# Performance work log

Hardware: AMD Instinct MI355X
Metric: run time of the kernel (lower is better)

## Reference

```python
import jax, jax.numpy as jnp
import numpy as np

B, S, C, HD = 1, 2048, 2048, 128
H = C // HD  # 16 heads
EPS = float(jnp.finfo(jnp.float32).eps)  # torch nn.RMSNorm default eps


def setup_inputs() -> dict:
    key = jax.random.key(0)
    ks = jax.random.split(key, 10)
    std = 1.0 / np.sqrt(C)
    return {
        "x": jax.random.normal(ks[0], (B, S, C), jnp.float32),
        "rope": jax.random.normal(ks[1], (1, S, 1, HD // 2, 2, 2), jnp.float32),
        "wq": jax.random.normal(ks[2], (C, C), jnp.float32) * std,
        "bq": jax.random.normal(ks[3], (C,), jnp.float32) * 0.01,
        "wk": jax.random.normal(ks[4], (C, C), jnp.float32) * std,
        "bk": jax.random.normal(ks[5], (C,), jnp.float32) * 0.01,
        "wv": jax.random.normal(ks[6], (C, C), jnp.float32) * std,
        "bv": jax.random.normal(ks[7], (C,), jnp.float32) * 0.01,
        "q_norm_w": jnp.ones((HD,), jnp.float32),
        "k_norm_w": jnp.ones((HD,), jnp.float32),
        "wo": jax.random.normal(ks[8], (C, C), jnp.float32) * std,
        "bo": jax.random.normal(ks[9], (C,), jnp.float32) * 0.01,
    }


def _rmsnorm(x, w):
    # x: [..., HD]
    ms = jnp.mean(x * x, axis=-1, keepdims=True)
    return x * jax.lax.rsqrt(ms + EPS) * w


def _apply_rotary(x, rope):
    # x: [B,S,H,HD]; rope: [1,S,1,HD//2,2,2]
    shp = x.shape
    x_ = x.reshape(*shp[:-1], -1, 1, 2)          # [B,S,H,HD/2,1,2]
    out = (rope * x_).sum(axis=-1)               # [B,S,H,HD/2,2]
    return out.reshape(shp)


def reference(x, rope, wq, bq, wk, bk, wv, bv, q_norm_w, k_norm_w, wo, bo):
    q = x @ wq.T + bq
    k = x @ wk.T + bk
    v = x @ wv.T + bv
    q = q.reshape(B, S, H, HD)
    k = k.reshape(B, S, H, HD)
    v = v.reshape(B, S, H, HD)
    q = _rmsnorm(q, q_norm_w)
    k = _rmsnorm(k, k_norm_w)
    q = _apply_rotary(q, rope)
    k = _apply_rotary(k, rope)
    scale = 1.0 / np.sqrt(HD)
    scores = jnp.einsum("bqhd,bkhd->bhqk", q, k) * scale  # [B,H,S,S]
    attn = jax.nn.softmax(scores, axis=-1)
    out = jnp.einsum("bhqk,bkhd->bqhd", attn, v).reshape(B, S, C)
    return out @ wo.T + bo
```

## Files before the change

### kernel.cpp

```cpp
#include <hip/hip_runtime.h>
#include <stdint.h>

#define GLOBAL_AS __attribute__((address_space(1)))
#define LDS_AS    __attribute__((address_space(3)))

typedef unsigned short u16;
typedef __attribute__((ext_vector_type(8))) __bf16 bf16x8;
typedef __attribute__((ext_vector_type(4))) float   f32x4;
typedef __attribute__((ext_vector_type(2))) float   f32x2;
typedef __attribute__((ext_vector_type(4))) u16     u16x4;

#if __has_builtin(__builtin_amdgcn_exp2f)
#define EXP2(x) __builtin_amdgcn_exp2f(x)
#else
#define EXP2(x) __exp2f(x)
#endif

static __device__ __forceinline__ float bf2f(u16 u) {
    union { uint32_t i; float f; } c; c.i = ((uint32_t)u) << 16; return c.f;
}
static __device__ __forceinline__ u16 f2bf(float f) {
    union { float f; uint32_t i; } c; c.f = f;
    uint32_t r = c.i + 0x7fffu + ((c.i >> 16) & 1u);
    return (u16)(r >> 16);
}
static __device__ __forceinline__ u16 f2bf_fast(float f) {
    union { float f; uint32_t i; } c; c.f = f;
    return (u16)((c.i + 0x8000u) >> 16);
}
static __device__ __forceinline__ void gl_lds16(const void* g, void* l) {
    __builtin_amdgcn_global_load_lds((GLOBAL_AS const uint32_t*)g,
                                     (LDS_AS uint32_t*)l, 16, 0, 0);
}
static __device__ __forceinline__ f32x4 mfma16(bf16x8 a, bf16x8 b, f32x4 c) {
    return __builtin_amdgcn_mfma_f32_16x16x32_bf16(a, b, c, 0, 0, 0);
}

__global__ __launch_bounds__(256) void cast5(
    const float* __restrict__ s0, const float* __restrict__ s1,
    const float* __restrict__ s2, const float* __restrict__ s3,
    const float* __restrict__ s4,
    u16* __restrict__ d0, u16* __restrict__ d1, u16* __restrict__ d2,
    u16* __restrict__ d3, u16* __restrict__ d4)
{
    const float* s; u16* d;
    switch (blockIdx.y) {
        case 0: s = s0; d = d0; break;
        case 1: s = s1; d = d1; break;
        case 2: s = s2; d = d2; break;
        case 3: s = s3; d = d3; break;
        default: s = s4; d = d4; break;
    }
    int i = (blockIdx.x * 256 + threadIdx.x) * 4;
    f32x4 v = *(const f32x4*)&s[i];
    u16x4 u = { f2bf(v[0]), f2bf(v[1]), f2bf(v[2]), f2bf(v[3]) };
    *(u16x4*)&d[i] = u;
}

__global__ __launch_bounds__(512, 2) void gemm_qkv7(
    const u16* __restrict__ x,
    const u16* __restrict__ wq, const u16* __restrict__ wk, const u16* __restrict__ wv,
    const float* __restrict__ bq, const float* __restrict__ bk, const float* __restrict__ bv,
    u16* __restrict__ q, u16* __restrict__ k, u16* __restrict__ v)
{
    __shared__ u16 SL[4][16384];
    const int tid = threadIdx.x, l = tid & 63, w = tid >> 6;
    const int wm = w >> 2, wn = w & 3;
    const int lr = l & 15, lg = l >> 4;
    const int lg2 = lg ^ ((lr >> 1) & 3);
    const int bid = blockIdx.x;
    const int bm = bid & 7, bn = bid >> 3;

    const u16* Ab = x + (size_t)(bm * 256) * 2048;

    const int uA0 = tid,       rA0 = uA0 >> 2, cA0 = (uA0 & 3) ^ ((rA0 >> 1) & 3);
    const int uA1 = 512 + tid, rA1 = uA1 >> 2, cA1 = (uA1 & 3) ^ ((rA1 >> 1) & 3);
    const u16* apA0 = Ab + (size_t)rA0 * 2048 + cA0 * 8;
    const u16* apA1 = Ab + (size_t)rA1 * 2048 + cA1 * 8;
    const int ub0 = tid;
    int ub1 = 512 + tid; if (ub1 > 767) ub1 = 767;
    const int rB0 = ub0 >> 2, cB0 = (ub0 & 3) ^ ((rB0 >> 1) & 3);
    const int rB1 = ub1 >> 2, cB1 = (ub1 & 3) ^ ((rB1 >> 1) & 3);
    const int gr0 = bn * 192 + rB0, gr1 = bn * 192 + rB1;
    const u16* base0 = gr0 < 2048 ? wq : (gr0 < 4096 ? wk : wv);
    const u16* base1 = gr1 < 2048 ? wq : (gr1 < 4096 ? wk : wv);
    const u16* bpB0 = base0 + (size_t)(gr0 & 2047) * 2048 + cB0 * 8;
    const u16* bpB1 = base1 + (size_t)(gr1 & 2047) * 2048 + cB1 * 8;
    const int dA0 = uA0 * 8, dA1 = uA1 * 8;
    const int dB0 = (1024 + tid) * 8, dB1 = (1536 + tid) * 8;

    auto stageA = [&](u16* slot) {
        gl_lds16(apA0, slot + dA0);
        gl_lds16(apA1, slot + dA1);
        apA0 += 32; apA1 += 32;
    };
    auto stageB = [&](u16* slot) {
        gl_lds16(bpB0, slot + dB0);
        gl_lds16(bpB1, slot + dB1);
        bpB0 += 32; bpB1 += 32;
    };

    f32x4 acc[8][3];
#pragma unroll
    for (int mi = 0; mi < 8; ++mi)
#pragma unroll
        for (int nj = 0; nj < 3; ++nj) acc[mi][nj] = (f32x4){0.f, 0.f, 0.f, 0.f};

    stageA((u16*)SL[0]); stageB((u16*)SL[0]);
    stageA((u16*)SL[1]); stageB((u16*)SL[1]);
    stageA((u16*)SL[2]); stageB((u16*)SL[2]);

    const int ar = wm * 128 + lr;
    const int br = wn * 48 + lr;

    auto iter_body = [&](const u16* As0, const u16* As1, u16* sl3, u16* sl4) {
        const u16* Bs0 = As0 + 8192;
        const u16* Bs1 = As1 + 8192;

        asm volatile("s_waitcnt vmcnt(4)" ::: "memory");
        __builtin_amdgcn_s_barrier();
        __builtin_amdgcn_sched_barrier(0);

        bf16x8 b0[3], alo0[4], ahi0[4], b1[3], alo1[4], ahi1[4];

        stageA(sl3);
#pragma unroll
        for (int nj = 0; nj < 3; ++nj)
            b0[nj] = *(const bf16x8*)&Bs0[(br + nj * 16) * 32 + lg2 * 8];
#pragma unroll
        for (int mi = 0; mi < 4; ++mi)
            alo0[mi] = *(const bf16x8*)&As0[(ar + mi * 16) * 32 + lg2 * 8];
#pragma unroll
        for (int mi = 0; mi < 4; ++mi)
            ahi0[mi] = *(const bf16x8*)&As0[(ar + (4 + mi) * 16) * 32 + lg2 * 8];
        __builtin_amdgcn_s_setprio(1);
#pragma unroll
        for (int mi = 0; mi < 4; ++mi)
#pragma unroll
            for (int nj = 0; nj < 3; ++nj)
                acc[mi][nj] = mfma16(alo0[mi], b0[nj], acc[mi][nj]);
        __builtin_amdgcn_s_setprio(0);

        stageB(sl3);
#pragma unroll
        for (int nj = 0; nj < 3; ++nj)
            b1[nj] = *(const bf16x8*)&Bs1[(br + nj * 16) * 32 + lg2 * 8];
#pragma unroll
        for (int mi = 0; mi < 4; ++mi)
            alo1[mi] = *(const bf16x8*)&As1[(ar + mi * 16) * 32 + lg2 * 8];
        __builtin_amdgcn_s_setprio(1);
#pragma unroll
        for (int mi = 0; mi < 4; ++mi)
#pragma unroll
            for (int nj = 0; nj < 3; ++nj)
                acc[4 + mi][nj] = mfma16(ahi0[mi], b0[nj], acc[4 + mi][nj]);
        __builtin_amdgcn_s_setprio(0);

        __builtin_amdgcn_sched_barrier(0);
        __builtin_amdgcn_s_barrier();
        __builtin_amdgcn_sched_barrier(0);

        stageA(sl4);
#pragma unroll
        for (int mi = 0; mi < 4; ++mi)
            ahi1[mi] = *(const bf16x8*)&As1[(ar + (4 + mi) * 16) * 32 + lg2 * 8];
        __builtin_amdgcn_s_setprio(1);
#pragma unroll
        for (int mi = 0; mi < 4; ++mi)
#pragma unroll
            for (int nj = 0; nj < 3; ++nj)
                acc[mi][nj] = mfma16(alo1[mi], b1[nj], acc[mi][nj]);
        __builtin_amdgcn_s_setprio(0);

        stageB(sl4);
        __builtin_amdgcn_s_setprio(1);
#pragma unroll
        for (int mi = 0; mi < 4; ++mi)
#pragma unroll
            for (int nj = 0; nj < 3; ++nj)
                acc[4 + mi][nj] = mfma16(ahi1[mi], b1[nj], acc[4 + mi][nj]);
        __builtin_amdgcn_s_setprio(0);
    };

#pragma unroll 1
    for (int it2 = 0; it2 < 16; ++it2) {
        iter_body((const u16*)SL[0], (const u16*)SL[1], (u16*)SL[3], (u16*)SL[0]);
        iter_body((const u16*)SL[2], (const u16*)SL[3], (u16*)SL[1], (u16*)SL[2]);
    }
    asm volatile("s_waitcnt vmcnt(0)" ::: "memory");

#pragma unroll
    for (int mi = 0; mi < 8; ++mi) {
        int row0 = bm * 256 + wm * 128 + mi * 16 + lg * 4;
#pragma unroll
        for (int nj = 0; nj < 3; ++nj) {
            int col = bn * 192 + wn * 48 + nj * 16 + lr;
            int cs = (col >> 11), cc = col & 2047;
            u16* C = cs == 0 ? q : (cs == 1 ? k : v);
            const float* bp = cs == 0 ? bq : (cs == 1 ? bk : bv);
            float bs = bp[cc];
#pragma unroll
            for (int reg = 0; reg < 4; ++reg)
                C[(size_t)(row0 + reg) * 2048 + cc] = f2bf(acc[mi][nj][reg] + bs);
        }
    }
}

__global__ __launch_bounds__(256, 2) void gemm_out4(
    const u16* __restrict__ a, const u16* __restrict__ wo,
    const float* __restrict__ bo, float* __restrict__ out)
{
    __shared__ u16 SL[4][8192];
    const int tid = threadIdx.x, l = tid & 63, w = tid >> 6;
    const int wm = w >> 1, wn = w & 1;
    const int lr = l & 15, lg = l >> 4;
    const int lg2 = lg ^ ((lr >> 1) & 3);
    const int bid = blockIdx.x;
    const int xcd = bid & 7, j = bid >> 3;
    const int bm = xcd * 2 + (j & 1), bn = j >> 1;

    const u16* Ab = a  + (size_t)(bm * 128) * 2048;
    const u16* Bb = wo + (size_t)(bn * 128) * 2048;

    const int r0 = tid >> 2,        c0 = (tid & 3) ^ ((r0 >> 1) & 3);
    const int r1 = (256 + tid) >> 2, c1 = ((256 + tid) & 3) ^ ((r1 >> 1) & 3);
    const u16* apA0 = Ab + (size_t)r0 * 2048 + c0 * 8;
    const u16* apA1 = Ab + (size_t)r1 * 2048 + c1 * 8;
    const u16* bpB0 = Bb + (size_t)r0 * 2048 + c0 * 8;
    const u16* bpB1 = Bb + (size_t)r1 * 2048 + c1 * 8;
    const int dA0 = tid * 8, dA1 = (256 + tid) * 8;
    const int dB0 = (512 + tid) * 8, dB1 = (768 + tid) * 8;

    auto stage = [&](u16* slot) {
        gl_lds16(apA0, slot + dA0);
        gl_lds16(apA1, slot + dA1);
        gl_lds16(bpB0, slot + dB0);
        gl_lds16(bpB1, slot + dB1);
        apA0 += 32; apA1 += 32; bpB0 += 32; bpB1 += 32;
    };

    f32x4 acc[4][4];
#pragma unroll
    for (int mi = 0; mi < 4; ++mi)
#pragma unroll
        for (int nj = 0; nj < 4; ++nj) acc[mi][nj] = (f32x4){0.f, 0.f, 0.f, 0.f};

    stage((u16*)SL[0]); stage((u16*)SL[1]); stage((u16*)SL[2]);

    auto ob = [&](const u16* As, u16* sln) {
        const u16* Bs = As + 4096;
        asm volatile("s_waitcnt vmcnt(8)" ::: "memory");
        __builtin_amdgcn_s_barrier();
        __builtin_amdgcn_sched_barrier(0);

        stage(sln);

        bf16x8 bf[4], af0[2];
#pragma unroll
        for (int nj = 0; nj < 4; ++nj)
            bf[nj] = *(const bf16x8*)&Bs[(wn * 64 + nj * 16 + lr) * 32 + lg2 * 8];
#pragma unroll
        for (int mi = 0; mi < 2; ++mi)
            af0[mi] = *(const bf16x8*)&As[(wm * 64 + mi * 16 + lr) * 32 + lg2 * 8];
        __builtin_amdgcn_s_setprio(1);
#pragma unroll
        for (int mi = 0; mi < 2; ++mi)
#pragma unroll
            for (int nj = 0; nj < 4; ++nj)
                acc[mi][nj] = mfma16(af0[mi], bf[nj], acc[mi][nj]);
        __builtin_amdgcn_s_setprio(0);
        __builtin_amdgcn_s_barrier();
        __builtin_amdgcn_sched_barrier(0);

        bf16x8 af1[2];
#pragma unroll
        for (int mi = 0; mi < 2; ++mi)
            af1[mi] = *(const bf16x8*)&As[(wm * 64 + (2 + mi) * 16 + lr) * 32 + lg2 * 8];
        __builtin_amdgcn_s_setprio(1);
#pragma unroll
        for (int mi = 0; mi < 2; ++mi)
#pragma unroll
            for (int nj = 0; nj < 4; ++nj)
                acc[2 + mi][nj] = mfma16(af1[mi], bf[nj], acc[2 + mi][nj]);
        __builtin_amdgcn_s_setprio(0);
    };

#pragma unroll 1
    for (int it4 = 0; it4 < 16; ++it4) {
        ob((const u16*)SL[0], (u16*)SL[3]);
        ob((const u16*)SL[1], (u16*)SL[0]);
        ob((const u16*)SL[2], (u16*)SL[1]);
        ob((const u16*)SL[3], (u16*)SL[2]);
    }
    asm volatile("s_waitcnt vmcnt(0)" ::: "memory");

#pragma unroll
    for (int mi = 0; mi < 4; ++mi) {
        int row0 = bm * 128 + wm * 64 + mi * 16 + lg * 4;
#pragma unroll
        for (int nj = 0; nj < 4; ++nj) {
            int col = bn * 128 + wn * 64 + nj * 16 + lr;
            float bs = bo[col];
#pragma unroll
            for (int reg = 0; reg < 4; ++reg)
                out[(size_t)(row0 + reg) * 2048 + col] = acc[mi][nj][reg] + bs;
        }
    }
}

__global__ __launch_bounds__(256) void norm_rope(
    const u16* __restrict__ qb, const u16* __restrict__ kb,
    const float* __restrict__ rope, const float* __restrict__ qw, const float* __restrict__ kw,
    u16* __restrict__ qh, u16* __restrict__ kh)
{
    const int tid = threadIdx.x, l = tid & 63, w = tid >> 6;
    const int rowid = blockIdx.x * 4 + w;
    const int h = rowid & 15, s = rowid >> 4;
    const size_t gbase = (size_t)s * 2048 + h * 128 + 2 * l;

    uint32_t qu = *(const uint32_t*)&qb[gbase];
    uint32_t ku = *(const uint32_t*)&kb[gbase];
    float q0 = bf2f((u16)qu), q1 = bf2f((u16)(qu >> 16));
    float k0 = bf2f((u16)ku), k1 = bf2f((u16)(ku >> 16));

    float sq = q0 * q0 + q1 * q1;
    float sk = k0 * k0 + k1 * k1;
#pragma unroll
    for (int m = 1; m < 64; m <<= 1) {
        sq += __shfl_xor(sq, m);
        sk += __shfl_xor(sk, m);
    }
    const float EPS = 1.1920928955078125e-07f;
    const float SCALE = 0.08838834764831845f * 1.4426950408889634f;
    float rq = rsqrtf(sq * (1.f / 128.f) + EPS) * SCALE;
    float rk = rsqrtf(sk * (1.f / 128.f) + EPS);

    f32x2 wq2 = *(const f32x2*)&qw[2 * l];
    f32x2 wk2 = *(const f32x2*)&kw[2 * l];
    float qn0 = q0 * rq * wq2[0], qn1 = q1 * rq * wq2[1];
    float kn0 = k0 * rk * wk2[0], kn1 = k1 * rk * wk2[1];

    f32x4 rr = *(const f32x4*)&rope[(size_t)s * 256 + l * 4];
    float qo0 = rr[0] * qn0 + rr[1] * qn1;
    float qo1 = rr[2] * qn0 + rr[3] * qn1;
    float ko0 = rr[0] * kn0 + rr[1] * kn1;
    float ko1 = rr[2] * kn0 + rr[3] * kn1;

    const size_t obase = ((size_t)h * 2048 + s) * 128 + 2 * l;
    *(uint32_t*)&qh[obase] = (uint32_t)f2bf(qo0) | ((uint32_t)f2bf(qo1) << 16);
    *(uint32_t*)&kh[obase] = (uint32_t)f2bf(ko0) | ((uint32_t)f2bf(ko1) << 16);
}

__global__ __launch_bounds__(256) void transpose_v(
    const u16* __restrict__ vb, u16* __restrict__ vt)
{
    __shared__ u16 t[64 * 80];
    const int h = blockIdx.z, s0 = blockIdx.x * 64, d0 = blockIdx.y * 64;
    const int tid = threadIdx.x;
#pragma unroll
    for (int cc = tid; cc < 512; cc += 256) {
        int r = cc >> 3, u = cc & 7;
        *(bf16x8*)&t[r * 80 + u * 8] =
            *(const bf16x8*)&vb[(size_t)(s0 + r) * 2048 + h * 128 + d0 + u * 8];
    }
    __syncthreads();
#pragma unroll
    for (int cc = tid; cc < 512; cc += 256) {
        int dr = cc >> 3, u = cc & 7;
        u16 vv[8];
#pragma unroll
        for (int j = 0; j < 8; ++j) vv[j] = t[(u * 8 + j) * 80 + dr];
        u16x4 lo = { vv[0], vv[1], vv[2], vv[3] };
        u16x4 hi = { vv[4], vv[5], vv[6], vv[7] };
        u16* dst = &vt[((size_t)h * 128 + d0 + dr) * 2048 + s0 + u * 8];
        *(u16x4*)dst = lo;
        *(u16x4*)(dst + 4) = hi;
    }
}

__global__ __launch_bounds__(256, 2) void attn(
    const u16* __restrict__ qh, const u16* __restrict__ kh,
    const u16* __restrict__ vt, u16* __restrict__ Opb, float* __restrict__ Lp)
{
    __shared__ u16 Ks[64 * 128];
    __shared__ u16 Vs[128 * 64];
    __shared__ u16 Ps[4][32 * 68];
    const int tid = threadIdx.x, l = tid & 63, w = tid >> 6;
    const int h = blockIdx.z, half = blockIdx.y;
    const int q0 = blockIdx.x * 128 + w * 32;
    const int lr = l & 15, lg = l >> 4;
    const float SHIFT = -17.312340490667562f;

    const u16* Kh = kh + (size_t)h * 2048 * 128;
    const u16* Vh = vt + (size_t)h * 128 * 2048;
    const int kvbase = half * 1024;

    bf16x8 qf[2][4];
#pragma unroll
    for (int am = 0; am < 2; ++am)
#pragma unroll
        for (int kk = 0; kk < 4; ++kk)
            qf[am][kk] = *(const bf16x8*)
                &qh[((size_t)h * 2048 + q0 + am * 16 + lr) * 128 + kk * 32 + lg * 8];

    bf16x8 onesf;
#pragma unroll
    for (int j = 0; j < 8; ++j) {
        union { u16 u; __bf16 b; } cb; cb.u = 0x3F80;
        onesf[j] = cb.b;
    }

    f32x4 o[2][8];
#pragma unroll
    for (int am = 0; am < 2; ++am)
#pragma unroll
        for (int dj = 0; dj < 8; ++dj) o[am][dj] = (f32x4){0.f, 0.f, 0.f, 0.f};
    f32x4 ol[2] = { (f32x4){0.f, 0.f, 0.f, 0.f}, (f32x4){0.f, 0.f, 0.f, 0.f} };

#pragma unroll 1
    for (int t = 0; t < 16; ++t) {
        const int kv0 = kvbase + t * 64;
        __syncthreads();
#pragma unroll
        for (int r = 0; r < 4; ++r) {
            int c = w * 4 + r;
            {
                int row = c * 4 + (l >> 4);
                int u = (l & 15) ^ (row & 7);
                gl_lds16(Kh + (size_t)(kv0 + row) * 128 + u * 8, &Ks[c * 512 + l * 8]);
            }
            {
                int row = c * 8 + (l >> 3);
                int u = (l & 7) ^ (row & 7);
                gl_lds16(Vh + (size_t)row * 2048 + kv0 + u * 8, &Vs[c * 512 + l * 8]);
            }
        }
        __syncthreads();

        f32x4 sc[2][4];
#pragma unroll
        for (int am = 0; am < 2; ++am)
#pragma unroll
            for (int nj = 0; nj < 4; ++nj)
                sc[am][nj] = (f32x4){SHIFT, SHIFT, SHIFT, SHIFT};
        __builtin_amdgcn_s_setprio(1);
#pragma unroll
        for (int kk = 0; kk < 4; ++kk)
#pragma unroll
            for (int nj = 0; nj < 4; ++nj) {
                int n = nj * 16 + lr;
                bf16x8 b = *(const bf16x8*)&Ks[n * 128 + ((kk * 4 + lg) ^ (n & 7)) * 8];
#pragma unroll
                for (int am = 0; am < 2; ++am)
                    sc[am][nj] = mfma16(qf[am][kk], b, sc[am][nj]);
            }
        __builtin_amdgcn_s_setprio(0);

#pragma unroll
        for (int am = 0; am < 2; ++am)
#pragma unroll
            for (int reg = 0; reg < 4; ++reg)
#pragma unroll
                for (int nj = 0; nj < 4; ++nj)
                    Ps[w][(am * 16 + lg * 4 + reg) * 68 + nj * 16 + lr] =
                        f2bf_fast(EXP2(sc[am][nj][reg]));
        asm volatile("s_waitcnt lgkmcnt(0)" ::: "memory");
        __builtin_amdgcn_sched_barrier(0);

        bf16x8 pa[2][2];
#pragma unroll
        for (int am = 0; am < 2; ++am)
#pragma unroll
            for (int kk2 = 0; kk2 < 2; ++kk2) {
                union { u16x4 h4[2]; bf16x8 v8; } cvt;
                cvt.h4[0] = *(const u16x4*)&Ps[w][(am * 16 + lr) * 68 + kk2 * 32 + lg * 8];
                cvt.h4[1] = *(const u16x4*)&Ps[w][(am * 16 + lr) * 68 + kk2 * 32 + lg * 8 + 4];
                pa[am][kk2] = cvt.v8;
            }
        __builtin_amdgcn_s_setprio(1);
#pragma unroll
        for (int am = 0; am < 2; ++am)
#pragma unroll
            for (int kk2 = 0; kk2 < 2; ++kk2)
                ol[am] = mfma16(pa[am][kk2], onesf, ol[am]);
#pragma unroll
        for (int dj = 0; dj < 8; ++dj)
#pragma unroll
            for (int kk2 = 0; kk2 < 2; ++kk2) {
                int n = dj * 16 + lr;
                bf16x8 b = *(const bf16x8*)&Vs[n * 64 + ((kk2 * 4 + lg) ^ (n & 7)) * 8];
#pragma unroll
                for (int am = 0; am < 2; ++am)
                    o[am][dj] = mfma16(pa[am][kk2], b, o[am][dj]);
            }
        __builtin_amdgcn_s_setprio(0);
    }

    if (lr == 0) {
#pragma unroll
        for (int am = 0; am < 2; ++am)
#pragma unroll
            for (int reg = 0; reg < 4; ++reg)
                Lp[(half * 16 + h) * 2048 + q0 + am * 16 + lg * 4 + reg] = ol[am][reg];
    }
#pragma unroll
    for (int am = 0; am < 2; ++am)
#pragma unroll
        for (int dj = 0; dj < 8; ++dj)
#pragma unroll
            for (int reg = 0; reg < 4; ++reg)
                Opb[((size_t)(half * 2048) + q0 + am * 16 + lg * 4 + reg) * 2048 +
                    h * 128 + dj * 16 + lr] = f2bf(o[am][dj][reg]);
}

__global__ __launch_bounds__(256) void combine(
    const u16* __restrict__ Opb, const float* __restrict__ Lp, u16* __restrict__ ab)
{
    int idx = (blockIdx.x * 256 + threadIdx.x) * 4;
    int s = idx >> 11, c = idx & 2047, h = c >> 7;
    u16x4 a4 = *(const u16x4*)&Opb[(size_t)s * 2048 + c];
    u16x4 b4 = *(const u16x4*)&Opb[(size_t)(2048 + s) * 2048 + c];
    float rl = 1.0f / (Lp[h * 2048 + s] + Lp[(16 + h) * 2048 + s]);
    u16x4 u = { f2bf((bf2f(a4[0]) + bf2f(b4[0])) * rl),
                f2bf((bf2f(a4[1]) + bf2f(b4[1])) * rl),
                f2bf((bf2f(a4[2]) + bf2f(b4[2])) * rl),
                f2bf((bf2f(a4[3]) + bf2f(b4[3])) * rl) };
    *(u16x4*)&ab[idx] = u;
}

extern "C" void kernel_launch(void* const* d_in, const int* in_sizes, int n_in,
                              void* d_out, int out_size, void* d_ws, size_t ws_size,
                              hipStream_t stream)
{
    (void)in_sizes; (void)n_in; (void)out_size;
    const float* x    = (const float*)d_in[0];
    const float* rope = (const float*)d_in[1];
    const float* wq   = (const float*)d_in[2];
    const float* bq   = (const float*)d_in[3];
    const float* wk   = (const float*)d_in[4];
    const float* bk   = (const float*)d_in[5];
    const float* wv   = (const float*)d_in[6];
    const float* bv   = (const float*)d_in[7];
    const float* qw   = (const float*)d_in[8];
    const float* kw   = (const float*)d_in[9];
    const float* wo   = (const float*)d_in[10];
    const float* bo   = (const float*)d_in[11];
    float* out = (float*)d_out;

    const size_t NE = 2048ull * 2048ull;
    if (ws_size < 13 * NE * 2) return;
    u16* p = (u16*)d_ws;
    u16* xb  = p; p += NE;
    u16* wqb = p; p += NE;
    u16* wkb = p; p += NE;
    u16* wvb = p; p += NE;
    u16* wob = p; p += NE;
    u16* qb  = p; p += NE;
    u16* kb  = p; p += NE;
    u16* vb  = p; p += NE;
    u16* qhb = p; p += NE;
    u16* khb = p; p += NE;
    u16* ab  = p; p += NE;
    u16* vtb = p; p += NE;
    u16* spare = p; p += NE;
    (void)spare;

    u16*   Opb = xb;
    float* Lp  = (float*)qb;

    cast5<<<dim3(4096, 5), 256, 0, stream>>>(x, wq, wk, wv, wo, xb, wqb, wkb, wvb, wob);
    gemm_qkv7<<<256, 512, 0, stream>>>(xb, wqb, wkb, wvb, bq, bk, bv, qb, kb, vb);
    norm_rope<<<8192, 256, 0, stream>>>(qb, kb, rope, qw, kw, qhb, khb);
    transpose_v<<<dim3(32, 2, 16), 256, 0, stream>>>(vb, vtb);
    attn<<<dim3(16, 2, 16), 256, 0, stream>>>(qhb, khb, vtb, Opb, Lp);
    combine<<<4096, 256, 0, stream>>>(Opb, Lp, ab);
    gemm_out4<<<256, 256, 0, stream>>>(ab, wob, bo, out);
}
```

Baseline: 163.8 us.

## Use 256x256 tiles per weight matrix in QKV GEMM with 192 blocks

Changes the fused QKV projection GEMM from 256x192 output tiles over the concatenated weights to 256x256 tiles that each lie within a single Q, K or V weight matrix. This removes per-element weight and bias selection and the uneven, clamped B-tile loads, and raises MFMA work per LDS fragment load. In exchange the grid drops from 256 to 192 blocks, so on a 256-CU device some CUs sit idle, and each wave holds more accumulator registers.

```diff
diff --git a/kernel.cpp b/kernel.cpp
--- a/kernel.cpp
+++ b/kernel.cpp
@@ -57,7 +57,7 @@
     *(u16x4*)&d[i] = u;
 }
 
-__global__ __launch_bounds__(512, 2) void gemm_qkv7(
+__global__ __launch_bounds__(512, 2) void gemm_qkv8(
     const u16* __restrict__ x,
     const u16* __restrict__ wq, const u16* __restrict__ wk, const u16* __restrict__ wv,
     const float* __restrict__ bq, const float* __restrict__ bk, const float* __restrict__ bv,
@@ -70,23 +70,21 @@
     const int lg2 = lg ^ ((lr >> 1) & 3);
     const int bid = blockIdx.x;
     const int bm = bid & 7, bn = bid >> 3;
+    const int wsel = bn >> 3, bnl = bn & 7;
+    const u16* W = (wsel == 0) ? wq : (wsel == 1) ? wk : wv;
+    const float* bias = (wsel == 0) ? bq : (wsel == 1) ? bk : bv;
+    u16* C = (wsel == 0) ? q : (wsel == 1) ? k : v;
 
     const u16* Ab = x + (size_t)(bm * 256) * 2048;
-
-    const int uA0 = tid,       rA0 = uA0 >> 2, cA0 = (uA0 & 3) ^ ((rA0 >> 1) & 3);
-    const int uA1 = 512 + tid, rA1 = uA1 >> 2, cA1 = (uA1 & 3) ^ ((rA1 >> 1) & 3);
-    const u16* apA0 = Ab + (size_t)rA0 * 2048 + cA0 * 8;
-    const u16* apA1 = Ab + (size_t)rA1 * 2048 + cA1 * 8;
-    const int ub0 = tid;
-    int ub1 = 512 + tid; if (ub1 > 767) ub1 = 767;
-    const int rB0 = ub0 >> 2, cB0 = (ub0 & 3) ^ ((rB0 >> 1) & 3);
-    const int rB1 = ub1 >> 2, cB1 = (ub1 & 3) ^ ((rB1 >> 1) & 3);
-    const int gr0 = bn * 192 + rB0, gr1 = bn * 192 + rB1;
-    const u16* base0 = gr0 < 2048 ? wq : (gr0 < 4096 ? wk : wv);
-    const u16* base1 = gr1 < 2048 ? wq : (gr1 < 4096 ? wk : wv);
-    const u16* bpB0 = base0 + (size_t)(gr0 & 2047) * 2048 + cB0 * 8;
-    const u16* bpB1 = base1 + (size_t)(gr1 & 2047) * 2048 + cB1 * 8;
-    const int dA0 = uA0 * 8, dA1 = uA1 * 8;
+    const u16* Bb = W + (size_t)(bnl * 256) * 2048;
+
+    const int r0 = tid >> 2,         c0 = (tid & 3) ^ ((r0 >> 1) & 3);
+    const int r1 = (512 + tid) >> 2, c1 = ((512 + tid) & 3) ^ ((r1 >> 1) & 3);
+    const u16* apA0 = Ab + (size_t)r0 * 2048 + c0 * 8;
+    const u16* apA1 = Ab + (size_t)r1 * 2048 + c1 * 8;
+    const u16* bpB0 = Bb + (size_t)r0 * 2048 + c0 * 8;
+    const u16* bpB1 = Bb + (size_t)r1 * 2048 + c1 * 8;
+    const int dA0 = tid * 8, dA1 = (512 + tid) * 8;
     const int dB0 = (1024 + tid) * 8, dB1 = (1536 + tid) * 8;
 
     auto stageA = [&](u16* slot) {
@@ -100,18 +98,18 @@
         bpB0 += 32; bpB1 += 32;
     };
 
-    f32x4 acc[8][3];
+    f32x4 acc[8][4];
 #pragma unroll
     for (int mi = 0; mi < 8; ++mi)
 #pragma unroll
-        for (int nj = 0; nj < 3; ++nj) acc[mi][nj] = (f32x4){0.f, 0.f, 0.f, 0.f};
+        for (int nj = 0; nj < 4; ++nj) acc[mi][nj] = (f32x4){0.f, 0.f, 0.f, 0.f};
 
     stageA((u16*)SL[0]); stageB((u16*)SL[0]);
     stageA((u16*)SL[1]); stageB((u16*)SL[1]);
     stageA((u16*)SL[2]); stageB((u16*)SL[2]);
 
     const int ar = wm * 128 + lr;
-    const int br = wn * 48 + lr;
+    const int br = wn * 64 + lr;
 
     auto iter_body = [&](const u16* As0, const u16* As1, u16* sl3, u16* sl4) {
         const u16* Bs0 = As0 + 8192;
@@ -121,11 +119,11 @@
         __builtin_amdgcn_s_barrier();
         __builtin_amdgcn_sched_barrier(0);
 
-        bf16x8 b0[3], alo0[4], ahi0[4], b1[3], alo1[4], ahi1[4];
+        bf16x8 b0[4], alo0[4], ahi0[4], b1[4], alo1[4], ahi1[4];
 
         stageA(sl3);
 #pragma unroll
-        for (int nj = 0; nj < 3; ++nj)
+        for (int nj = 0; nj < 4; ++nj)
             b0[nj] = *(const bf16x8*)&Bs0[(br + nj * 16) * 32 + lg2 * 8];
 #pragma unroll
         for (int mi = 0; mi < 4; ++mi)
@@ -137,13 +135,13 @@
 #pragma unroll
         for (int mi = 0; mi < 4; ++mi)
 #pragma unroll
-            for (int nj = 0; nj < 3; ++nj)
+            for (int nj = 0; nj < 4; ++nj)
                 acc[mi][nj] = mfma16(alo0[mi], b0[nj], acc[mi][nj]);
         __builtin_amdgcn_s_setprio(0);
 
         stageB(sl3);
 #pragma unroll
-        for (int nj = 0; nj < 3; ++nj)
+        for (int nj = 0; nj < 4; ++nj)
             b1[nj] = *(const bf16x8*)&Bs1[(br + nj * 16) * 32 + lg2 * 8];
 #pragma unroll
         for (int mi = 0; mi < 4; ++mi)
@@ -152,7 +150,7 @@
 #pragma unroll
         for (int mi = 0; mi < 4; ++mi)
 #pragma unroll
-            for (int nj = 0; nj < 3; ++nj)
+            for (int nj = 0; nj < 4; ++nj)
                 acc[4 + mi][nj] = mfma16(ahi0[mi], b0[nj], acc[4 + mi][nj]);
         __builtin_amdgcn_s_setprio(0);
 
@@ -168,7 +166,7 @@
 #pragma unroll
         for (int mi = 0; mi < 4; ++mi)
 #pragma unroll
-            for (int nj = 0; nj < 3; ++nj)
+            for (int nj = 0; nj < 4; ++nj)
                 acc[mi][nj] = mfma16(alo1[mi], b1[nj], acc[mi][nj]);
         __builtin_amdgcn_s_setprio(0);
 
@@ -177,7 +175,7 @@
 #pragma unroll
         for (int mi = 0; mi < 4; ++mi)
 #pragma unroll
-            for (int nj = 0; nj < 3; ++nj)
+            for (int nj = 0; nj < 4; ++nj)
                 acc[4 + mi][nj] = mfma16(ahi1[mi], b1[nj], acc[4 + mi][nj]);
         __builtin_amdgcn_s_setprio(0);
     };
@@ -193,12 +191,9 @@
     for (int mi = 0; mi < 8; ++mi) {
         int row0 = bm * 256 + wm * 128 + mi * 16 + lg * 4;
 #pragma unroll
-        for (int nj = 0; nj < 3; ++nj) {
-            int col = bn * 192 + wn * 48 + nj * 16 + lr;
-            int cs = (col >> 11), cc = col & 2047;
-            u16* C = cs == 0 ? q : (cs == 1 ? k : v);
-            const float* bp = cs == 0 ? bq : (cs == 1 ? bk : bv);
-            float bs = bp[cc];
+        for (int nj = 0; nj < 4; ++nj) {
+            int cc = bnl * 256 + wn * 64 + nj * 16 + lr;
+            float bs = bias[cc];
 #pragma unroll
             for (int reg = 0; reg < 4; ++reg)
                 C[(size_t)(row0 + reg) * 2048 + cc] = f2bf(acc[mi][nj][reg] + bs);
@@ -569,7 +564,7 @@
     float* Lp  = (float*)qb;
 
     cast5<<<dim3(4096, 5), 256, 0, stream>>>(x, wq, wk, wv, wo, xb, wqb, wkb, wvb, wob);
-    gemm_qkv7<<<256, 512, 0, stream>>>(xb, wqb, wkb, wvb, bq, bk, bv, qb, kb, vb);
+    gemm_qkv8<<<192, 512, 0, stream>>>(xb, wqb, wkb, wvb, bq, bk, bv, qb, kb, vb);
     norm_rope<<<8192, 256, 0, stream>>>(qb, kb, rope, qw, kw, qhb, khb);
     transpose_v<<<dim3(32, 2, 16), 256, 0, stream>>>(vb, vtb);
     attn<<<dim3(16, 2, 16), 256, 0, stream>>>(qhb, khb, vtb, Opb, Lp);
```

New measurement: 161.3 us. About the same (-1.5%).

## Fuse V transpose into QKV GEMM epilogue and widen output GEMM to 512 threads

Applied to the files above, without the earlier changes.

The QKV GEMM epilogue now writes V directly in transposed [h*128+d][s] layout as packed 4-element stores, so the separate transpose_v kernel and its extra read/write pass over V are removed. The output projection GEMM is switched from 256 to 512 threads per block with 8 waves, each computing a 64x32 sub-tile and issuing one A and one B async load per stage instead of two each. The transposed V stores are strided by 2048 elements and may coalesce less well, and smaller per-wave tiles lower MFMA reuse per LDS read in the output GEMM.

```diff
diff --git a/kernel.cpp b/kernel.cpp
--- a/kernel.cpp
+++ b/kernel.cpp
@@ -61,7 +61,7 @@
     const u16* __restrict__ x,
     const u16* __restrict__ wq, const u16* __restrict__ wk, const u16* __restrict__ wv,
     const float* __restrict__ bq, const float* __restrict__ bk, const float* __restrict__ bv,
-    u16* __restrict__ q, u16* __restrict__ k, u16* __restrict__ v)
+    u16* __restrict__ q, u16* __restrict__ k, u16* __restrict__ vt)
 {
     __shared__ u16 SL[4][16384];
     const int tid = threadIdx.x, l = tid & 63, w = tid >> 6;
@@ -196,23 +196,29 @@
         for (int nj = 0; nj < 3; ++nj) {
             int col = bn * 192 + wn * 48 + nj * 16 + lr;
             int cs = (col >> 11), cc = col & 2047;
-            u16* C = cs == 0 ? q : (cs == 1 ? k : v);
             const float* bp = cs == 0 ? bq : (cs == 1 ? bk : bv);
             float bs = bp[cc];
-#pragma unroll
-            for (int reg = 0; reg < 4; ++reg)
-                C[(size_t)(row0 + reg) * 2048 + cc] = f2bf(acc[mi][nj][reg] + bs);
+            if (cs == 2) {
+                u16x4 pk = { f2bf(acc[mi][nj][0] + bs), f2bf(acc[mi][nj][1] + bs),
+                             f2bf(acc[mi][nj][2] + bs), f2bf(acc[mi][nj][3] + bs) };
+                *(u16x4*)&vt[(size_t)cc * 2048 + row0] = pk;
+            } else {
+                u16* C = cs == 0 ? q : k;
+#pragma unroll
+                for (int reg = 0; reg < 4; ++reg)
+                    C[(size_t)(row0 + reg) * 2048 + cc] = f2bf(acc[mi][nj][reg] + bs);
+            }
         }
     }
 }
 
-__global__ __launch_bounds__(256, 2) void gemm_out4(
+__global__ __launch_bounds__(512, 2) void gemm_out5(
     const u16* __restrict__ a, const u16* __restrict__ wo,
     const float* __restrict__ bo, float* __restrict__ out)
 {
     __shared__ u16 SL[4][8192];
     const int tid = threadIdx.x, l = tid & 63, w = tid >> 6;
-    const int wm = w >> 1, wn = w & 1;
+    const int wm = w >> 2, wn = w & 3;
     const int lr = l & 15, lg = l >> 4;
     const int lg2 = lg ^ ((lr >> 1) & 3);
     const int bid = blockIdx.x;
@@ -222,43 +228,37 @@
     const u16* Ab = a  + (size_t)(bm * 128) * 2048;
     const u16* Bb = wo + (size_t)(bn * 128) * 2048;
 
-    const int r0 = tid >> 2,        c0 = (tid & 3) ^ ((r0 >> 1) & 3);
-    const int r1 = (256 + tid) >> 2, c1 = ((256 + tid) & 3) ^ ((r1 >> 1) & 3);
-    const u16* apA0 = Ab + (size_t)r0 * 2048 + c0 * 8;
-    const u16* apA1 = Ab + (size_t)r1 * 2048 + c1 * 8;
-    const u16* bpB0 = Bb + (size_t)r0 * 2048 + c0 * 8;
-    const u16* bpB1 = Bb + (size_t)r1 * 2048 + c1 * 8;
-    const int dA0 = tid * 8, dA1 = (256 + tid) * 8;
-    const int dB0 = (512 + tid) * 8, dB1 = (768 + tid) * 8;
+    const int r0 = tid >> 2, c0 = (tid & 3) ^ ((r0 >> 1) & 3);
+    const u16* apA = Ab + (size_t)r0 * 2048 + c0 * 8;
+    const u16* bpB = Bb + (size_t)r0 * 2048 + c0 * 8;
+    const int dA = tid * 8, dB = (512 + tid) * 8;
 
     auto stage = [&](u16* slot) {
-        gl_lds16(apA0, slot + dA0);
-        gl_lds16(apA1, slot + dA1);
-        gl_lds16(bpB0, slot + dB0);
-        gl_lds16(bpB1, slot + dB1);
-        apA0 += 32; apA1 += 32; bpB0 += 32; bpB1 += 32;
+        gl_lds16(apA, slot + dA);
+        gl_lds16(bpB, slot + dB);
+        apA += 32; bpB += 32;
     };
 
-    f32x4 acc[4][4];
+    f32x4 acc[4][2];
 #pragma unroll
     for (int mi = 0; mi < 4; ++mi)
 #pragma unroll
-        for (int nj = 0; nj < 4; ++nj) acc[mi][nj] = (f32x4){0.f, 0.f, 0.f, 0.f};
+        for (int nj = 0; nj < 2; ++nj) acc[mi][nj] = (f32x4){0.f, 0.f, 0.f, 0.f};
 
     stage((u16*)SL[0]); stage((u16*)SL[1]); stage((u16*)SL[2]);
 
     auto ob = [&](const u16* As, u16* sln) {
         const u16* Bs = As + 4096;
-        asm volatile("s_waitcnt vmcnt(8)" ::: "memory");
+        asm volatile("s_waitcnt vmcnt(4)" ::: "memory");
         __builtin_amdgcn_s_barrier();
         __builtin_amdgcn_sched_barrier(0);
 
         stage(sln);
 
-        bf16x8 bf[4], af0[2];
-#pragma unroll
-        for (int nj = 0; nj < 4; ++nj)
-            bf[nj] = *(const bf16x8*)&Bs[(wn * 64 + nj * 16 + lr) * 32 + lg2 * 8];
+        bf16x8 bf[2], af0[2];
+#pragma unroll
+        for (int nj = 0; nj < 2; ++nj)
+            bf[nj] = *(const bf16x8*)&Bs[(wn * 32 + nj * 16 + lr) * 32 + lg2 * 8];
 #pragma unroll
         for (int mi = 0; mi < 2; ++mi)
             af0[mi] = *(const bf16x8*)&As[(wm * 64 + mi * 16 + lr) * 32 + lg2 * 8];
@@ -266,7 +266,7 @@
 #pragma unroll
         for (int mi = 0; mi < 2; ++mi)
 #pragma unroll
-            for (int nj = 0; nj < 4; ++nj)
+            for (int nj = 0; nj < 2; ++nj)
                 acc[mi][nj] = mfma16(af0[mi], bf[nj], acc[mi][nj]);
         __builtin_amdgcn_s_setprio(0);
         __builtin_amdgcn_s_barrier();
@@ -280,7 +280,7 @@
 #pragma unroll
         for (int mi = 0; mi < 2; ++mi)
 #pragma unroll
-            for (int nj = 0; nj < 4; ++nj)
+            for (int nj = 0; nj < 2; ++nj)
                 acc[2 + mi][nj] = mfma16(af1[mi], bf[nj], acc[2 + mi][nj]);
         __builtin_amdgcn_s_setprio(0);
     };
@@ -298,8 +298,8 @@
     for (int mi = 0; mi < 4; ++mi) {
         int row0 = bm * 128 + wm * 64 + mi * 16 + lg * 4;
 #pragma unroll
-        for (int nj = 0; nj < 4; ++nj) {
-            int col = bn * 128 + wn * 64 + nj * 16 + lr;
+        for (int nj = 0; nj < 2; ++nj) {
+            int col = bn * 128 + wn * 32 + nj * 16 + lr;
             float bs = bo[col];
 #pragma unroll
             for (int reg = 0; reg < 4; ++reg)
@@ -349,33 +349,6 @@
     const size_t obase = ((size_t)h * 2048 + s) * 128 + 2 * l;
     *(uint32_t*)&qh[obase] = (uint32_t)f2bf(qo0) | ((uint32_t)f2bf(qo1) << 16);
     *(uint32_t*)&kh[obase] = (uint32_t)f2bf(ko0) | ((uint32_t)f2bf(ko1) << 16);
-}
-
-__global__ __launch_bounds__(256) void transpose_v(
-    const u16* __restrict__ vb, u16* __restrict__ vt)
-{
-    __shared__ u16 t[64 * 80];
-    const int h = blockIdx.z, s0 = blockIdx.x * 64, d0 = blockIdx.y * 64;
-    const int tid = threadIdx.x;
-#pragma unroll
-    for (int cc = tid; cc < 512; cc += 256) {
-        int r = cc >> 3, u = cc & 7;
-        *(bf16x8*)&t[r * 80 + u * 8] =
-            *(const bf16x8*)&vb[(size_t)(s0 + r) * 2048 + h * 128 + d0 + u * 8];
-    }
-    __syncthreads();
-#pragma unroll
-    for (int cc = tid; cc < 512; cc += 256) {
-        int dr = cc >> 3, u = cc & 7;
-        u16 vv[8];
-#pragma unroll
-        for (int j = 0; j < 8; ++j) vv[j] = t[(u * 8 + j) * 80 + dr];
-        u16x4 lo = { vv[0], vv[1], vv[2], vv[3] };
-        u16x4 hi = { vv[4], vv[5], vv[6], vv[7] };
-        u16* dst = &vt[((size_t)h * 128 + d0 + dr) * 2048 + s0 + u * 8];
-        *(u16x4*)dst = lo;
-        *(u16x4*)(dst + 4) = hi;
-    }
 }
 
 __global__ __launch_bounds__(256, 2) void attn(
@@ -563,16 +536,15 @@
     u16* ab  = p; p += NE;
     u16* vtb = p; p += NE;
     u16* spare = p; p += NE;
-    (void)spare;
+    (void)spare; (void)vb;
 
     u16*   Opb = xb;
     float* Lp  = (float*)qb;
 
     cast5<<<dim3(4096, 5), 256, 0, stream>>>(x, wq, wk, wv, wo, xb, wqb, wkb, wvb, wob);
-    gemm_qkv7<<<256, 512, 0, stream>>>(xb, wqb, wkb, wvb, bq, bk, bv, qb, kb, vb);
+    gemm_qkv7<<<256, 512, 0, stream>>>(xb, wqb, wkb, wvb, bq, bk, bv, qb, kb, vtb);
     norm_rope<<<8192, 256, 0, stream>>>(qb, kb, rope, qw, kw, qhb, khb);
-    transpose_v<<<dim3(32, 2, 16), 256, 0, stream>>>(vb, vtb);
     attn<<<dim3(16, 2, 16), 256, 0, stream>>>(qhb, khb, vtb, Opb, Lp);
     combine<<<4096, 256, 0, stream>>>(Opb, Lp, ab);
-    gemm_out4<<<256, 256, 0, stream>>>(ab, wob, bo, out);
-}
+    gemm_out5<<<256, 512, 0, stream>>>(ab, wob, bo, out);
+}
```

Result: faster. 158.9 us (-3.0%).
